# Kernel optimization log

Measured on AMD Instinct MI355X. Metric: run time of the kernel, lower is better.

The kernel has to match this reference:

```python
import jax, jax.numpy as jnp
import numpy as np

B, S, H = 2, 1024, 2048
KD = 32
N_CACHE = 16
RANKS = (4, 12, 40, 128)
SIM_THRESH = 0.95
CRIT_T, SIMPLE_T = 0.8, 0.3
EPS = 1e-8


def setup_inputs() -> dict:
    key = jax.random.key(0)
    ks = jax.random.split(key, 24)
    f32 = jnp.float32
    inp = {}
    inp['hidden_states'] = jax.random.normal(ks[0], (B, S, H), f32)
    # token importance scorer: Linear(H, H//4) -> ReLU -> Linear(H//4, 1)
    inp['scorer_w1'] = jax.random.normal(ks[1], (H // 4, H), f32) * 0.1
    inp['scorer_b1'] = jnp.zeros((H // 4,), f32)
    inp['scorer_w2'] = jax.random.normal(ks[2], (1, H // 4), f32) * 0.1
    inp['scorer_b2'] = jnp.zeros((1,), f32)
    inp['pos_importance'] = jnp.ones((1024,), f32)
    # orthogonal key projection [KD, H] (rows orthonormal)
    q, _ = jnp.linalg.qr(jax.random.normal(ks[3], (H, KD), f32))
    inp['key_proj_w'] = q.T
    # cached keys: per-batch-row L2-normalized then flattened, as in _compute_key
    ck = jax.random.normal(ks[4], (N_CACHE, B, KD), f32)
    ck = ck / jnp.linalg.norm(ck, axis=-1, keepdims=True)
    inp['cache_keys'] = ck.reshape(N_CACHE, B * KD)
    inp['cache_deltas'] = jax.random.normal(ks[5], (N_CACHE, B, S, H), f32) * 0.02
    # complexity estimator: Linear(H, 64) -> ReLU -> Linear(64, 4)
    inp['ce_w1'] = jax.random.normal(ks[6], (64, H), f32) * 0.02
    inp['ce_b1'] = jnp.zeros((64,), f32)
    inp['ce_w2'] = jax.random.normal(ks[7], (len(RANKS), 64), f32) * 0.02
    inp['ce_b2'] = jnp.zeros((len(RANKS),), f32)
    # adaptive low-rank U/V per rank option, init std=0.02
    for i, r in enumerate(RANKS):
        inp[f'u{r}'] = jax.random.normal(ks[8 + 2 * i], (r, H), f32) * 0.02
        inp[f'v{r}'] = jax.random.normal(ks[9 + 2 * i], (H, r), f32) * 0.02
    # dense stand-in for the wrapped original transformer layer
    inp['layer_w'] = jax.random.normal(ks[16], (H, H), f32) * 0.02
    inp['layer_b'] = jnp.zeros((H,), f32)
    return inp


def _forward(hidden_states, scorer_w1, scorer_b1, scorer_w2, scorer_b2,
             pos_importance, key_proj_w, cache_keys, cache_deltas,
             ce_w1, ce_b1, ce_w2, ce_b2,
             u4, v4, u12, v12, u40, v40, u128, v128,
             layer_w, layer_b):
    x = hidden_states
    Bn, Sn, _ = x.shape
    # ---- token importance scoring ----
    h = jax.nn.relu(jnp.einsum('bsh,fh->bsf', x, scorer_w1) + scorer_b1)
    content = jnp.einsum('bsf,of->bso', h, scorer_w2)[..., 0] + scorer_b2[0]  # [B,S]
    pos = pos_importance[:Sn][None, :]
    imp = jax.nn.sigmoid(content + 0.1 * pos)
    imp = imp.at[:, 0].multiply(2.0).at[:, -1].multiply(2.0)
    critical = imp > CRIT_T
    simple = imp < SIMPLE_T
    normal = ~(critical | simple)
    # ---- critical path: original layer on critically-masked input ----
    crit_in = jnp.where(critical[..., None], x, 0.0)
    crit_out = jnp.einsum('bsh,oh->bso', crit_in, layer_w) + layer_b
    # ---- simple path: batched 1-NN cosine cache lookup (replaces python loop) ----
    x_pooled = x.mean(axis=1)  # [B,H]
    qk = jax.lax.stop_gradient(x_pooled @ key_proj_w.T)  # no_grad in original
    qk = qk / jnp.maximum(jnp.linalg.norm(qk, axis=-1, keepdims=True), EPS)
    qf = qk.reshape(-1)  # flattened [B*KD], as F.cosine_similarity(dim=0)
    ck = jax.lax.stop_gradient(cache_keys)  # cached entries are detached
    sims = (ck @ qf) / (jnp.maximum(jnp.linalg.norm(ck, axis=-1), EPS)
                        * jnp.maximum(jnp.linalg.norm(qf), EPS))  # [N_CACHE]
    best = jnp.argmax(sims)
    hit = sims[best] >= SIM_THRESH
    cached_delta = jax.lax.stop_gradient(cache_deltas[best])  # [B,S,H]
    lr4 = (x @ u4.T) @ v4.T  # rank-4 update on cache miss
    simple_out = x + jnp.where(hit, cached_delta, lr4)
    # ---- normal path: adaptive-rank low-rank update ----
    ce_h = jax.nn.relu(jax.lax.stop_gradient(x_pooled) @ ce_w1.T + ce_b1)
    scores = ce_h @ ce_w2.T + ce_b2  # [B,4]
    rank_idx = jnp.argmax(scores.reshape(-1)) % len(RANKS)  # flat argmax as torch.argmax
    branches = [
        lambda xx: (xx @ u4.T) @ v4.T,
        lambda xx: (xx @ u12.T) @ v12.T,
        lambda xx: (xx @ u40.T) @ v40.T,
        lambda xx: (xx @ u128.T) @ v128.T,
    ]
    normal_update = jax.lax.switch(rank_idx, branches, x)
    normal_out = x + normal_update
    # ---- route per-token (masks partition all tokens) ----
    out = jnp.where(critical[..., None], crit_out,
          jnp.where(simple[..., None], simple_out, normal_out))
    return out


def reference(hidden_states, scorer_w1, scorer_b1, scorer_w2, scorer_b2,
              pos_importance, key_proj_w, cache_keys, cache_deltas,
              ce_w1, ce_b1, ce_w2, ce_b2,
              u4, v4, u12, v12, u40, v40, u128, v128,
              layer_w, layer_b):
    return _forward(hidden_states, scorer_w1, scorer_b1, scorer_w2, scorer_b2,
                    pos_importance, key_proj_w, cache_keys, cache_deltas,
                    ce_w1, ce_b1, ce_w2, ce_b2,
                    u4, v4, u12, v12, u40, v40, u128, v128,
                    layer_w, layer_b)
```

## Files before the change

### kernel.cpp

```cpp
#include <hip/hip_runtime.h>
#include <math.h>

#define B_  2
#define S_  1024
#define H_  2048
#define F_  512
#define KD_ 32
#define NC_ 16
#define M_  2048
#define NPROJ 184
#define LDP 192
#define KZ_ 4

typedef __attribute__((ext_vector_type(8))) short bf16x8;
typedef __attribute__((ext_vector_type(4))) float f32x4;

typedef __attribute__((address_space(1))) const void gvoid_t;
typedef __attribute__((address_space(3))) void lvoid_t;

__device__ __forceinline__ void gld16(const void* g, void* l) {
    __builtin_amdgcn_global_load_lds((gvoid_t*)g, (lvoid_t*)l, 16, 0, 0);
}

__device__ __forceinline__ ushort f2bf(float f) {
    unsigned u = __float_as_uint(f);
    u += 0x7FFFu + ((u >> 16) & 1u);
    return (ushort)(u >> 16);
}
__device__ __forceinline__ float bf2f(ushort h) {
    return __uint_as_float(((unsigned)h) << 16);
}
__device__ __forceinline__ uint4 pack_hi8(float4 a, float4 b) {
    uint4 r;
    r.x = (unsigned)f2bf(a.x) | ((unsigned)f2bf(a.y) << 16);
    r.y = (unsigned)f2bf(a.z) | ((unsigned)f2bf(a.w) << 16);
    r.z = (unsigned)f2bf(b.x) | ((unsigned)f2bf(b.y) << 16);
    r.w = (unsigned)f2bf(b.z) | ((unsigned)f2bf(b.w) << 16);
    return r;
}
__device__ __forceinline__ void pack_hilo8(float4 a, float4 b, uint4* hi, uint4* lo) {
    float v[8] = {a.x, a.y, a.z, a.w, b.x, b.y, b.z, b.w};
    unsigned h[8], l[8];
#pragma unroll
    for (int i = 0; i < 8; ++i) {
        ushort hh = f2bf(v[i]);
        h[i] = hh;
        l[i] = f2bf(v[i] - bf2f(hh));
    }
    *hi = make_uint4(h[0] | (h[1] << 16), h[2] | (h[3] << 16),
                     h[4] | (h[5] << 16), h[6] | (h[7] << 16));
    *lo = make_uint4(l[0] | (l[1] << 16), l[2] | (l[3] << 16),
                     l[4] | (l[5] << 16), l[6] | (l[7] << 16));
}

__global__ __launch_bounds__(256) void conv_kernel(
    const float* __restrict__ x, const float* __restrict__ lw,
    const float* __restrict__ sw1,
    const float* __restrict__ u4, const float* __restrict__ u12,
    const float* __restrict__ u40, const float* __restrict__ u128,
    ushort* __restrict__ xhi, ushort* __restrict__ xlo,
    ushort* __restrict__ lwh, ushort* __restrict__ swh,
    ushort* __restrict__ swl, ushort* __restrict__ ubh,
    float* __restrict__ partial) {
    int blk = blockIdx.x, tid = threadIdx.x;
    if (blk < 128) {
        int c0 = tid << 3;
        float cs0 = 0.f, cs1 = 0.f, cs2 = 0.f, cs3 = 0.f;
        float cs4 = 0.f, cs5 = 0.f, cs6 = 0.f, cs7 = 0.f;
        for (int r = 0; r < 16; ++r) {
            size_t off = (size_t)(blk * 16 + r) * H_ + c0;
            float4 a = *(const float4*)(x + off);
            float4 b = *(const float4*)(x + off + 4);
            cs0 += a.x; cs1 += a.y; cs2 += a.z; cs3 += a.w;
            cs4 += b.x; cs5 += b.y; cs6 += b.z; cs7 += b.w;
            uint4 hi, lo;
            pack_hilo8(a, b, &hi, &lo);
            *(uint4*)(xhi + off) = hi;
            *(uint4*)(xlo + off) = lo;
        }
        float* pr = partial + (size_t)blk * H_ + c0;
        pr[0] = cs0; pr[1] = cs1; pr[2] = cs2; pr[3] = cs3;
        pr[4] = cs4; pr[5] = cs5; pr[6] = cs6; pr[7] = cs7;
    } else if (blk < 1152) {
        size_t base = (size_t)(blk - 128) * 4096 + (size_t)tid * 16;
#pragma unroll
        for (int q = 0; q < 2; ++q) {
            size_t o = base + q * 8;
            float4 a = *(const float4*)(lw + o);
            float4 b = *(const float4*)(lw + o + 4);
            *(uint4*)(lwh + o) = pack_hi8(a, b);
        }
    } else if (blk < 1408) {
        size_t base = (size_t)(blk - 1152) * 4096 + (size_t)tid * 16;
#pragma unroll
        for (int q = 0; q < 2; ++q) {
            size_t o = base + q * 8;
            float4 a = *(const float4*)(sw1 + o);
            float4 b = *(const float4*)(sw1 + o + 4);
            uint4 hi, lo;
            pack_hilo8(a, b, &hi, &lo);
            *(uint4*)(swh + o) = hi;
            *(uint4*)(swl + o) = lo;
        }
    } else {
        const float* src; ushort* dst; int rel;
        if (blk < 1410)      { src = u4;   dst = ubh;            rel = blk - 1408; }
        else if (blk < 1416) { src = u12;  dst = ubh + 4 * H_;   rel = blk - 1410; }
        else if (blk < 1436) { src = u40;  dst = ubh + 16 * H_;  rel = blk - 1416; }
        else                 { src = u128; dst = ubh + 56 * H_;  rel = blk - 1436; }
        size_t base = (size_t)rel * 4096 + (size_t)tid * 16;
#pragma unroll
        for (int q = 0; q < 2; ++q) {
            size_t o = base + q * 8;
            float4 a = *(const float4*)(src + o);
            float4 b = *(const float4*)(src + o + 4);
            *(uint4*)(dst + o) = pack_hi8(a, b);
        }
    }
}

__global__ __launch_bounds__(256) void pool_final_kernel(
    const float* __restrict__ partial, float* __restrict__ xp) {
    int b = blockIdx.x >> 3, chunk = blockIdx.x & 7;
    int col = (chunk << 8) + threadIdx.x;
    float s = 0.f;
    for (int seg = 0; seg < 64; ++seg)
        s += partial[(size_t)(b * 64 + seg) * H_ + col];
    xp[b * H_ + col] = s * (1.0f / S_);
}

__global__ __launch_bounds__(256) void decide_dots(
    const float* __restrict__ xp, const float* __restrict__ kpw,
    const float* __restrict__ cw1, float* __restrict__ dots) {
    __shared__ float red[4];
    int o = blockIdx.x, tid = threadIdx.x;
    const float* xr;
    const float* wr;
    if (o < 64) {
        xr = xp + (o >> 5) * H_;
        wr = kpw + (size_t)(o & 31) * H_;
    } else {
        int o2 = o - 64;
        xr = xp + (o2 >> 6) * H_;
        wr = cw1 + (size_t)(o2 & 63) * H_;
    }
    int k0 = tid << 3;
    float4 xa = *(const float4*)(xr + k0);
    float4 xb = *(const float4*)(xr + k0 + 4);
    float4 wa = *(const float4*)(wr + k0);
    float4 wb = *(const float4*)(wr + k0 + 4);
    float s = xa.x * wa.x + xa.y * wa.y + xa.z * wa.z + xa.w * wa.w
            + xb.x * wb.x + xb.y * wb.y + xb.z * wb.z + xb.w * wb.w;
    for (int off = 32; off > 0; off >>= 1) s += __shfl_down(s, off, 64);
    if ((tid & 63) == 0) red[tid >> 6] = s;
    __syncthreads();
    if (tid == 0) dots[o] = red[0] + red[1] + red[2] + red[3];
}

__global__ __launch_bounds__(64) void decide_final(
    const float* __restrict__ dots, const float* __restrict__ ck,
    const float* __restrict__ cb1, const float* __restrict__ cw2,
    const float* __restrict__ cb2, int* __restrict__ flags) {
    __shared__ float qk_s[64], ce_s[128], sims_s[NC_], sc_s[8];
    __shared__ float qn_s;
    int tid = threadIdx.x;
    if (tid < 64) qk_s[tid] = dots[tid];
    if (tid < 64) {
        ce_s[tid]      = fmaxf(dots[64 + tid] + cb1[tid & 63], 0.f);
        ce_s[tid + 64] = fmaxf(dots[128 + tid] + cb1[tid & 63], 0.f);
    }
    __syncthreads();
    if (tid == 0) {
        for (int b = 0; b < B_; ++b) {
            float nn = 0.f;
            for (int d = 0; d < KD_; ++d) { float v = qk_s[b * KD_ + d]; nn += v * v; }
            float den = fmaxf(sqrtf(nn), 1e-8f);
            for (int d = 0; d < KD_; ++d) qk_s[b * KD_ + d] /= den;
        }
        float qn = 0.f;
        for (int i = 0; i < B_ * KD_; ++i) qn += qk_s[i] * qk_s[i];
        qn_s = fmaxf(sqrtf(qn), 1e-8f);
    }
    __syncthreads();
    if (tid < NC_) {
        float dot = 0.f, nn = 0.f;
        for (int i = 0; i < B_ * KD_; ++i) {
            float c = ck[tid * (B_ * KD_) + i];
            dot += c * qk_s[i]; nn += c * c;
        }
        sims_s[tid] = dot / (fmaxf(sqrtf(nn), 1e-8f) * qn_s);
    }
    if (tid >= 32 && tid < 40) {
        int p = tid - 32, b = p >> 2, o = p & 3;
        float v = cb2[o];
        for (int j = 0; j < 64; ++j) v += ce_s[b * 64 + j] * cw2[o * 64 + j];
        sc_s[p] = v;
    }
    __syncthreads();
    if (tid == 0) {
        float bestv = -1e30f; int best = 0;
        for (int n = 0; n < NC_; ++n)
            if (sims_s[n] > bestv) { bestv = sims_s[n]; best = n; }
        flags[2] = (bestv >= 0.95f) ? 1 : 0;
        flags[3] = best;
        float bs = -1e30f; int bi = 0;
        for (int p = 0; p < 8; ++p)
            if (sc_s[p] > bs) { bs = sc_s[p]; bi = p; }
        flags[1] = bi & 3;
    }
}

__global__ __launch_bounds__(256) void big_gemm(
    const ushort* __restrict__ xhi, const ushort* __restrict__ xlo,
    const ushort* __restrict__ swh, const ushort* __restrict__ swl,
    const ushort* __restrict__ ubh,
    float* __restrict__ Hp, float* __restrict__ Pp) {
    __shared__ ushort Ah[2][128][32], Al[2][128][32], Bh[2][128][32], Bl[2][128][32];
    int m0 = blockIdx.x << 7;
    int ny = blockIdx.y;
    int kz = blockIdx.z;
    bool split = ny < 4;
    int tid = threadIdx.x;
    int lr = tid >> 2;
    int lc = (tid & 3) << 3;

    const ushort* a0p = xhi + (size_t)(m0 + lr) * H_ + lc;
    const ushort* a1p = a0p + (size_t)64 * H_;
    const ushort* l0p = xlo + (size_t)(m0 + lr) * H_ + lc;
    const ushort* l1p = l0p + (size_t)64 * H_;
    const ushort* b0p; const ushort* b1p;
    const ushort* c0p = l0p; const ushort* c1p = l1p;
    if (split) {
        b0p = swh + (size_t)(ny * 128 + lr) * H_ + lc;
        b1p = b0p + (size_t)64 * H_;
        c0p = swl + (size_t)(ny * 128 + lr) * H_ + lc;
        c1p = c0p + (size_t)64 * H_;
    } else {
        b0p = ubh + (size_t)((ny - 4) * 128 + lr) * H_ + lc;
        b1p = b0p + (size_t)64 * H_;
    }

    int lane = tid & 63, w = tid >> 6;
    int wm = (w >> 1) << 6, wn = (w & 1) << 6;
    int fr = lane & 15, kb = (lane >> 4) << 3;

    f32x4 zero4 = {0.f, 0.f, 0.f, 0.f};
    f32x4 acc[4][4];
#pragma unroll
    for (int i = 0; i < 4; ++i)
#pragma unroll
        for (int j = 0; j < 4; ++j) acc[i][j] = zero4;

    int kbeg = kz << 9;

#define STAGE_BG(bb, k0)                                                  \
    do {                                                                  \
        gld16(a0p + (k0), &Ah[bb][lr][lc]);                               \
        gld16(a1p + (k0), &Ah[bb][lr + 64][lc]);                          \
        gld16(b0p + (k0), &Bh[bb][lr][lc]);                               \
        gld16(b1p + (k0), &Bh[bb][lr + 64][lc]);                          \
        if (split) {                                                      \
            gld16(l0p + (k0), &Al[bb][lr][lc]);                           \
            gld16(l1p + (k0), &Al[bb][lr + 64][lc]);                      \
            gld16(c0p + (k0), &Bl[bb][lr][lc]);                           \
            gld16(c1p + (k0), &Bl[bb][lr + 64][lc]);                      \
        }                                                                 \
    } while (0)

    STAGE_BG(0, kbeg);
    __syncthreads();
    int cur = 0;
    for (int kt = 0; kt < 16; ++kt) {
        if (kt + 1 < 16) STAGE_BG(cur ^ 1, kbeg + ((kt + 1) << 5));
        bf16x8 ah[4], bh4[4], al4[4], bl4[4];
#pragma unroll
        for (int mt = 0; mt < 4; ++mt)
            ah[mt] = *(const bf16x8*)&Ah[cur][wm + (mt << 4) + fr][kb];
#pragma unroll
        for (int nt = 0; nt < 4; ++nt)
            bh4[nt] = *(const bf16x8*)&Bh[cur][wn + (nt << 4) + fr][kb];
        if (split) {
#pragma unroll
            for (int mt = 0; mt < 4; ++mt)
                al4[mt] = *(const bf16x8*)&Al[cur][wm + (mt << 4) + fr][kb];
#pragma unroll
            for (int nt = 0; nt < 4; ++nt)
                bl4[nt] = *(const bf16x8*)&Bl[cur][wn + (nt << 4) + fr][kb];
        }
#pragma unroll
        for (int mt = 0; mt < 4; ++mt)
#pragma unroll
            for (int nt = 0; nt < 4; ++nt) {
                acc[mt][nt] = __builtin_amdgcn_mfma_f32_16x16x32_bf16(
                    ah[mt], bh4[nt], acc[mt][nt], 0, 0, 0);
                if (split) {
                    acc[mt][nt] = __builtin_amdgcn_mfma_f32_16x16x32_bf16(
                        ah[mt], bl4[nt], acc[mt][nt], 0, 0, 0);
                    acc[mt][nt] = __builtin_amdgcn_mfma_f32_16x16x32_bf16(
                        al4[mt], bh4[nt], acc[mt][nt], 0, 0, 0);
                }
            }
        __syncthreads();
        cur ^= 1;
    }
#undef STAGE_BG

    int orr = (lane >> 4) << 2;
    if (split) {
        float* dst = Hp + (size_t)kz * M_ * F_;
#pragma unroll
        for (int mt = 0; mt < 4; ++mt)
#pragma unroll
            for (int r = 0; r < 4; ++r) {
                int m = m0 + wm + (mt << 4) + orr + r;
                float* cr = dst + (size_t)m * F_ + (ny << 7) + wn;
#pragma unroll
                for (int nt = 0; nt < 4; ++nt)
                    cr[(nt << 4) + fr] = acc[mt][nt][r];
            }
    } else {
        float* dst = Pp + (size_t)kz * M_ * LDP;
        int nb0 = (ny - 4) << 7;
#pragma unroll
        for (int mt = 0; mt < 4; ++mt)
#pragma unroll
            for (int r = 0; r < 4; ++r) {
                int m = m0 + wm + (mt << 4) + orr + r;
                float* cr = dst + (size_t)m * LDP;
#pragma unroll
                for (int nt = 0; nt < 4; ++nt) {
                    int c = nb0 + wn + (nt << 4) + fr;
                    if (c < NPROJ) cr[c] = acc[mt][nt][r];
                }
            }
    }
}

__global__ __launch_bounds__(256) void route_kernel(
    const float* __restrict__ Hp, const float* __restrict__ sb1,
    const float* __restrict__ sw2, const float* __restrict__ sb2,
    const float* __restrict__ pos,
    int* __restrict__ flags, int* __restrict__ route, int* __restrict__ clist) {
    int tid = threadIdx.x;
    int m = (blockIdx.x << 2) + (tid >> 6);
    int lane = tid & 63;
    const float* h0 = Hp + (size_t)m * F_;
    const float* h1 = h0 + (size_t)M_ * F_;
    const float* h2 = h1 + (size_t)M_ * F_;
    const float* h3 = h2 + (size_t)M_ * F_;
    float s = 0.f;
    for (int f = lane; f < F_; f += 64)
        s += fmaxf(h0[f] + h1[f] + h2[f] + h3[f] + sb1[f], 0.f) * sw2[f];
    for (int off = 32; off > 0; off >>= 1) s += __shfl_down(s, off, 64);
    if (lane == 0) {
        float content = s + sb2[0];
        int si = m & (S_ - 1);
        float imp = 1.0f / (1.0f + expf(-(content + 0.1f * pos[si])));
        if (si == 0 || si == S_ - 1) imp *= 2.0f;
        int rt = (imp > 0.8f) ? 0 : ((imp < 0.3f) ? 1 : 2);
        route[m] = rt;
        if (rt == 0) {
            int idx = atomicAdd(&flags[0], 1);
            clist[idx] = m;
        }
    }
}

__global__ __launch_bounds__(256) void crit_gemm(
    const ushort* __restrict__ xhi, const ushort* __restrict__ lwh,
    const float* __restrict__ lb, const int* __restrict__ clist,
    const int* __restrict__ flags, float* __restrict__ out) {
    __shared__ ushort Ah[2][128][32], Bh[2][128][32];
    int M = flags[0];
    int m0 = blockIdx.x << 7;
    if (m0 >= M) return;
    int n0 = blockIdx.y << 7;
    int tid = threadIdx.x;
    int lr = tid >> 2, lc = (tid & 3) << 3;

    int gm0 = m0 + lr, gm1 = m0 + lr + 64;
    int ar0 = clist[gm0 < M ? gm0 : (M - 1)];
    int ar1 = clist[gm1 < M ? gm1 : (M - 1)];
    const ushort* a0p = xhi + (size_t)ar0 * H_ + lc;
    const ushort* a1p = xhi + (size_t)ar1 * H_ + lc;
    const ushort* b0p = lwh + (size_t)(n0 + lr) * H_ + lc;
    const ushort* b1p = b0p + (size_t)64 * H_;

    int lane = tid & 63, w = tid >> 6;
    int wm = (w >> 1) << 6, wn = (w & 1) << 6;
    int fr = lane & 15, kb = (lane >> 4) << 3;

    f32x4 zero4 = {0.f, 0.f, 0.f, 0.f};
    f32x4 acc[4][4];
#pragma unroll
    for (int i = 0; i < 4; ++i)
#pragma unroll
        for (int j = 0; j < 4; ++j) acc[i][j] = zero4;

#define STAGE_CG(bb, k0)                                                  \
    do {                                                                  \
        gld16(a0p + (k0), &Ah[bb][lr][lc]);                               \
        gld16(a1p + (k0), &Ah[bb][lr + 64][lc]);                          \
        gld16(b0p + (k0), &Bh[bb][lr][lc]);                               \
        gld16(b1p + (k0), &Bh[bb][lr + 64][lc]);                          \
    } while (0)

    STAGE_CG(0, 0);
    __syncthreads();
    int cur = 0;
    for (int kt = 0; kt < 64; ++kt) {
        if (kt + 1 < 64) STAGE_CG(cur ^ 1, (kt + 1) << 5);
        bf16x8 af[4], bf4[4];
#pragma unroll
        for (int mt = 0; mt < 4; ++mt)
            af[mt] = *(const bf16x8*)&Ah[cur][wm + (mt << 4) + fr][kb];
#pragma unroll
        for (int nt = 0; nt < 4; ++nt)
            bf4[nt] = *(const bf16x8*)&Bh[cur][wn + (nt << 4) + fr][kb];
#pragma unroll
        for (int mt = 0; mt < 4; ++mt)
#pragma unroll
            for (int nt = 0; nt < 4; ++nt)
                acc[mt][nt] = __builtin_amdgcn_mfma_f32_16x16x32_bf16(
                    af[mt], bf4[nt], acc[mt][nt], 0, 0, 0);
        __syncthreads();
        cur ^= 1;
    }
#undef STAGE_CG

    int orr = (lane >> 4) << 2;
#pragma unroll
    for (int mt = 0; mt < 4; ++mt)
#pragma unroll
        for (int r = 0; r < 4; ++r) {
            int m = m0 + wm + (mt << 4) + orr + r;
            if (m < M) {
                float* cr = out + (size_t)clist[m] * H_;
#pragma unroll
                for (int nt = 0; nt < 4; ++nt) {
                    int c = n0 + wn + (nt << 4) + fr;
                    cr[c] = acc[mt][nt][r] + lb[c];
                }
            }
        }
}

__global__ __launch_bounds__(256) void stage2_kernel(
    const float* __restrict__ x, const float* __restrict__ Pp,
    const float* __restrict__ v4, const float* __restrict__ v12,
    const float* __restrict__ v40, const float* __restrict__ v128,
    const float* __restrict__ cd, const int* __restrict__ flags,
    const int* __restrict__ route, float* __restrict__ out) {
    __shared__ float TsR[16][132];
    __shared__ float Ts4[16][4];
    __shared__ int rt_s[16];
    int tid = threadIdx.x;
    int m0 = (blockIdx.x >> 4) << 4;
    int c0 = (blockIdx.x & 15) << 7;

    if (tid < 16) rt_s[tid] = route[m0 + tid];
    int r = flags[1];
    const float* V = (r == 0) ? v4 : (r == 1) ? v12 : (r == 2) ? v40 : v128;
    int Kr  = (r == 0) ? 4 : (r == 1) ? 12 : (r == 2) ? 40 : 128;
    int off = (r == 0) ? 0 : (r == 1) ? 4  : (r == 2) ? 16 : 56;
    int hit = flags[2], best = flags[3];

    const float* Pp1 = Pp + (size_t)M_ * LDP;
    const float* Pp2 = Pp1 + (size_t)M_ * LDP;
    const float* Pp3 = Pp2 + (size_t)M_ * LDP;
    for (int idx = tid; idx < 16 * Kr; idx += 256) {
        int i = idx / Kr, j = idx - i * Kr;
        size_t o = (size_t)(m0 + i) * LDP + off + j;
        TsR[i][j] = Pp[o] + Pp1[o] + Pp2[o] + Pp3[o];
    }
    if (tid < 64) {
        int i = tid >> 2, j = tid & 3;
        size_t o = (size_t)(m0 + i) * LDP + j;
        Ts4[i][j] = Pp[o] + Pp1[o] + Pp2[o] + Pp3[o];
    }
    __syncthreads();
    bool any1 = false, any2 = false;
#pragma unroll
    for (int i = 0; i < 16; ++i) { any1 |= (rt_s[i] == 1); any2 |= (rt_s[i] == 2); }
    if (!any1 && !any2) return;
    bool need4 = any1 && !hit;

    int c = c0 + (tid & 127);
    int i0 = (tid >> 7) << 3;

    float aR[8];
#pragma unroll
    for (int i = 0; i < 8; ++i) aR[i] = 0.f;
    if (any2) {
        const float* vrow = V + (size_t)c * Kr;
        for (int j = 0; j < Kr; j += 4) {
            const float4 vv = *(const float4*)(vrow + j);
#pragma unroll
            for (int i = 0; i < 8; ++i) {
                const float4 tv = *(const float4*)&TsR[i0 + i][j];
                aR[i] += tv.x * vv.x + tv.y * vv.y + tv.z * vv.z + tv.w * vv.w;
            }
        }
    }
    float a4[8];
    if (need4) {
        const float4 vv = *(const float4*)(v4 + (size_t)c * 4);
#pragma unroll
        for (int i = 0; i < 8; ++i) {
            const float4 tv = *(const float4*)&Ts4[i0 + i][0];
            a4[i] = tv.x * vv.x + tv.y * vv.y + tv.z * vv.z + tv.w * vv.w;
        }
    }
#pragma unroll
    for (int i = 0; i < 8; ++i) {
        int rt = rt_s[i0 + i];
        if (rt == 0) continue;
        size_t o = (size_t)(m0 + i0 + i) * H_ + c;
        float upd;
        if (rt == 1)
            upd = hit ? cd[(size_t)best * (size_t)(M_ * H_) + o] : a4[i];
        else
            upd = aR[i];
        out[o] = x[o] + upd;
    }
}

extern "C" void kernel_launch(void* const* d_in, const int* in_sizes, int n_in,
                              void* d_out, int out_size, void* d_ws, size_t ws_size,
                              hipStream_t stream) {
    const float* x    = (const float*)d_in[0];
    const float* sw1  = (const float*)d_in[1];
    const float* sb1  = (const float*)d_in[2];
    const float* sw2  = (const float*)d_in[3];
    const float* sb2  = (const float*)d_in[4];
    const float* pos  = (const float*)d_in[5];
    const float* kpw  = (const float*)d_in[6];
    const float* ck   = (const float*)d_in[7];
    const float* cd   = (const float*)d_in[8];
    const float* cw1  = (const float*)d_in[9];
    const float* cb1  = (const float*)d_in[10];
    const float* cw2  = (const float*)d_in[11];
    const float* cb2  = (const float*)d_in[12];
    const float* u4   = (const float*)d_in[13];
    const float* v4   = (const float*)d_in[14];
    const float* u12  = (const float*)d_in[15];
    const float* v12  = (const float*)d_in[16];
    const float* u40  = (const float*)d_in[17];
    const float* v40  = (const float*)d_in[18];
    const float* u128 = (const float*)d_in[19];
    const float* v128 = (const float*)d_in[20];
    const float* lw   = (const float*)d_in[21];
    const float* lb   = (const float*)d_in[22];
    float* out = (float*)d_out;

    ushort* xhi = (ushort*)d_ws;
    ushort* xlo = xhi + (size_t)M_ * H_;
    ushort* lwh = xlo + (size_t)M_ * H_;
    ushort* swh = lwh + (size_t)H_ * H_;
    ushort* swl = swh + (size_t)F_ * H_;
    ushort* ubh = swl + (size_t)F_ * H_;
    float* fbase   = (float*)(ubh + (size_t)256 * H_);
    float* xp      = fbase;
    float* partial = xp + 2 * H_;
    float* Pp      = partial + 128 * H_;
    float* Hp      = Pp + (size_t)KZ_ * M_ * LDP;
    float* dots    = Hp + (size_t)KZ_ * M_ * F_;
    int*   flags   = (int*)(dots + 256);
    int*   route   = flags + 8;
    int*   clist   = route + M_;

    hipMemsetAsync(flags, 0, sizeof(int), stream);

    conv_kernel<<<1500, 256, 0, stream>>>(x, lw, sw1, u4, u12, u40, u128,
                                          xhi, xlo, lwh, swh, swl, ubh, partial);
    pool_final_kernel<<<16, 256, 0, stream>>>(partial, xp);
    decide_dots<<<192, 256, 0, stream>>>(xp, kpw, cw1, dots);
    decide_final<<<1, 64, 0, stream>>>(dots, ck, cb1, cw2, cb2, flags);
    big_gemm<<<dim3(16, 6, KZ_), 256, 0, stream>>>(xhi, xlo, swh, swl, ubh, Hp, Pp);
    route_kernel<<<512, 256, 0, stream>>>(Hp, sb1, sw2, sb2, pos,
                                          flags, route, clist);
    crit_gemm<<<dim3(16, 16), 256, 0, stream>>>(xhi, lwh, lb, clist, flags, out);
    stage2_kernel<<<2048, 256, 0, stream>>>(x, Pp, v4, v12, v40, v128,
                                            cd, flags, route, out);
}
```

Measured before the change: 519.0 us.

## Merge small decision kernels and fuse crit GEMM with stage2; swizzle LDS

Folds the pooling reduction into the dot-product kernel and moves the single-block decision logic into an extra block of the routing kernel. The critical-token GEMM and the stage2 update now run as one launch, with blocks split by index and sharing one shared-memory buffer. This cuts the launch count from eight to five and lets the two output-writing phases overlap. It also adds an XOR swizzle to the LDS column index in both GEMMs to reduce bank conflicts on the MFMA fragment reads. Each pooldots block now re-reads the full partial-sum buffer, so that redundant traffic is the cost.

Measured after the change: 479.6 us. 1.08x faster.

```diff
diff --git a/kernel.cpp b/kernel.cpp
--- a/kernel.cpp
+++ b/kernel.cpp
@@ -119,95 +119,41 @@
     }
 }
 
-__global__ __launch_bounds__(256) void pool_final_kernel(
-    const float* __restrict__ partial, float* __restrict__ xp) {
-    int b = blockIdx.x >> 3, chunk = blockIdx.x & 7;
-    int col = (chunk << 8) + threadIdx.x;
-    float s = 0.f;
-    for (int seg = 0; seg < 64; ++seg)
-        s += partial[(size_t)(b * 64 + seg) * H_ + col];
-    xp[b * H_ + col] = s * (1.0f / S_);
-}
-
-__global__ __launch_bounds__(256) void decide_dots(
-    const float* __restrict__ xp, const float* __restrict__ kpw,
+__global__ __launch_bounds__(256) void pooldots_kernel(
+    const float* __restrict__ partial, const float* __restrict__ kpw,
     const float* __restrict__ cw1, float* __restrict__ dots) {
     __shared__ float red[4];
     int o = blockIdx.x, tid = threadIdx.x;
-    const float* xr;
-    const float* wr;
+    int b; const float* wr;
     if (o < 64) {
-        xr = xp + (o >> 5) * H_;
+        b = o >> 5;
         wr = kpw + (size_t)(o & 31) * H_;
     } else {
         int o2 = o - 64;
-        xr = xp + (o2 >> 6) * H_;
+        b = o2 >> 6;
         wr = cw1 + (size_t)(o2 & 63) * H_;
     }
     int k0 = tid << 3;
-    float4 xa = *(const float4*)(xr + k0);
-    float4 xb = *(const float4*)(xr + k0 + 4);
+    float xs0 = 0.f, xs1 = 0.f, xs2 = 0.f, xs3 = 0.f;
+    float xs4 = 0.f, xs5 = 0.f, xs6 = 0.f, xs7 = 0.f;
+    const float* pb = partial + (size_t)b * 64 * H_ + k0;
+    for (int seg = 0; seg < 64; ++seg) {
+        float4 p0 = *(const float4*)(pb + (size_t)seg * H_);
+        float4 p1 = *(const float4*)(pb + (size_t)seg * H_ + 4);
+        xs0 += p0.x; xs1 += p0.y; xs2 += p0.z; xs3 += p0.w;
+        xs4 += p1.x; xs5 += p1.y; xs6 += p1.z; xs7 += p1.w;
+    }
+    const float inv = 1.0f / S_;
     float4 wa = *(const float4*)(wr + k0);
     float4 wb = *(const float4*)(wr + k0 + 4);
-    float s = xa.x * wa.x + xa.y * wa.y + xa.z * wa.z + xa.w * wa.w
-            + xb.x * wb.x + xb.y * wb.y + xb.z * wb.z + xb.w * wb.w;
+    float s = (xs0 * inv) * wa.x + (xs1 * inv) * wa.y
+            + (xs2 * inv) * wa.z + (xs3 * inv) * wa.w
+            + (xs4 * inv) * wb.x + (xs5 * inv) * wb.y
+            + (xs6 * inv) * wb.z + (xs7 * inv) * wb.w;
     for (int off = 32; off > 0; off >>= 1) s += __shfl_down(s, off, 64);
     if ((tid & 63) == 0) red[tid >> 6] = s;
     __syncthreads();
     if (tid == 0) dots[o] = red[0] + red[1] + red[2] + red[3];
-}
-
-__global__ __launch_bounds__(64) void decide_final(
-    const float* __restrict__ dots, const float* __restrict__ ck,
-    const float* __restrict__ cb1, const float* __restrict__ cw2,
-    const float* __restrict__ cb2, int* __restrict__ flags) {
-    __shared__ float qk_s[64], ce_s[128], sims_s[NC_], sc_s[8];
-    __shared__ float qn_s;
-    int tid = threadIdx.x;
-    if (tid < 64) qk_s[tid] = dots[tid];
-    if (tid < 64) {
-        ce_s[tid]      = fmaxf(dots[64 + tid] + cb1[tid & 63], 0.f);
-        ce_s[tid + 64] = fmaxf(dots[128 + tid] + cb1[tid & 63], 0.f);
-    }
-    __syncthreads();
-    if (tid == 0) {
-        for (int b = 0; b < B_; ++b) {
-            float nn = 0.f;
-            for (int d = 0; d < KD_; ++d) { float v = qk_s[b * KD_ + d]; nn += v * v; }
-            float den = fmaxf(sqrtf(nn), 1e-8f);
-            for (int d = 0; d < KD_; ++d) qk_s[b * KD_ + d] /= den;
-        }
-        float qn = 0.f;
-        for (int i = 0; i < B_ * KD_; ++i) qn += qk_s[i] * qk_s[i];
-        qn_s = fmaxf(sqrtf(qn), 1e-8f);
-    }
-    __syncthreads();
-    if (tid < NC_) {
-        float dot = 0.f, nn = 0.f;
-        for (int i = 0; i < B_ * KD_; ++i) {
-            float c = ck[tid * (B_ * KD_) + i];
-            dot += c * qk_s[i]; nn += c * c;
-        }
-        sims_s[tid] = dot / (fmaxf(sqrtf(nn), 1e-8f) * qn_s);
-    }
-    if (tid >= 32 && tid < 40) {
-        int p = tid - 32, b = p >> 2, o = p & 3;
-        float v = cb2[o];
-        for (int j = 0; j < 64; ++j) v += ce_s[b * 64 + j] * cw2[o * 64 + j];
-        sc_s[p] = v;
-    }
-    __syncthreads();
-    if (tid == 0) {
-        float bestv = -1e30f; int best = 0;
-        for (int n = 0; n < NC_; ++n)
-            if (sims_s[n] > bestv) { bestv = sims_s[n]; best = n; }
-        flags[2] = (bestv >= 0.95f) ? 1 : 0;
-        flags[3] = best;
-        float bs = -1e30f; int bi = 0;
-        for (int p = 0; p < 8; ++p)
-            if (sc_s[p] > bs) { bs = sc_s[p]; bi = p; }
-        flags[1] = bi & 3;
-    }
 }
 
 __global__ __launch_bounds__(256) void big_gemm(
@@ -223,26 +169,28 @@
     int tid = threadIdx.x;
     int lr = tid >> 2;
     int lc = (tid & 3) << 3;
-
-    const ushort* a0p = xhi + (size_t)(m0 + lr) * H_ + lc;
+    int lcs = lc ^ (((lr >> 1) & 3) << 3);
+
+    const ushort* a0p = xhi + (size_t)(m0 + lr) * H_ + lcs;
     const ushort* a1p = a0p + (size_t)64 * H_;
-    const ushort* l0p = xlo + (size_t)(m0 + lr) * H_ + lc;
+    const ushort* l0p = xlo + (size_t)(m0 + lr) * H_ + lcs;
     const ushort* l1p = l0p + (size_t)64 * H_;
     const ushort* b0p; const ushort* b1p;
     const ushort* c0p = l0p; const ushort* c1p = l1p;
     if (split) {
-        b0p = swh + (size_t)(ny * 128 + lr) * H_ + lc;
+        b0p = swh + (size_t)(ny * 128 + lr) * H_ + lcs;
         b1p = b0p + (size_t)64 * H_;
-        c0p = swl + (size_t)(ny * 128 + lr) * H_ + lc;
+        c0p = swl + (size_t)(ny * 128 + lr) * H_ + lcs;
         c1p = c0p + (size_t)64 * H_;
     } else {
-        b0p = ubh + (size_t)((ny - 4) * 128 + lr) * H_ + lc;
+        b0p = ubh + (size_t)((ny - 4) * 128 + lr) * H_ + lcs;
         b1p = b0p + (size_t)64 * H_;
     }
 
     int lane = tid & 63, w = tid >> 6;
     int wm = (w >> 1) << 6, wn = (w & 1) << 6;
-    int fr = lane & 15, kb = (lane >> 4) << 3;
+    int fr = lane & 15;
+    int kb = ((lane >> 4) << 3) ^ (((fr >> 1) & 3) << 3);
 
     f32x4 zero4 = {0.f, 0.f, 0.f, 0.f};
     f32x4 acc[4][4];
@@ -336,127 +284,186 @@
     }
 }
 
-__global__ __launch_bounds__(256) void route_kernel(
+__global__ __launch_bounds__(256) void routefinal_kernel(
     const float* __restrict__ Hp, const float* __restrict__ sb1,
     const float* __restrict__ sw2, const float* __restrict__ sb2,
     const float* __restrict__ pos,
+    const float* __restrict__ dots, const float* __restrict__ ck,
+    const float* __restrict__ cb1, const float* __restrict__ cw2,
+    const float* __restrict__ cb2,
     int* __restrict__ flags, int* __restrict__ route, int* __restrict__ clist) {
     int tid = threadIdx.x;
-    int m = (blockIdx.x << 2) + (tid >> 6);
-    int lane = tid & 63;
-    const float* h0 = Hp + (size_t)m * F_;
-    const float* h1 = h0 + (size_t)M_ * F_;
-    const float* h2 = h1 + (size_t)M_ * F_;
-    const float* h3 = h2 + (size_t)M_ * F_;
-    float s = 0.f;
-    for (int f = lane; f < F_; f += 64)
-        s += fmaxf(h0[f] + h1[f] + h2[f] + h3[f] + sb1[f], 0.f) * sw2[f];
-    for (int off = 32; off > 0; off >>= 1) s += __shfl_down(s, off, 64);
-    if (lane == 0) {
-        float content = s + sb2[0];
-        int si = m & (S_ - 1);
-        float imp = 1.0f / (1.0f + expf(-(content + 0.1f * pos[si])));
-        if (si == 0 || si == S_ - 1) imp *= 2.0f;
-        int rt = (imp > 0.8f) ? 0 : ((imp < 0.3f) ? 1 : 2);
-        route[m] = rt;
-        if (rt == 0) {
-            int idx = atomicAdd(&flags[0], 1);
-            clist[idx] = m;
-        }
-    }
-}
-
-__global__ __launch_bounds__(256) void crit_gemm(
+    if (blockIdx.x < 512) {
+        int m = ((int)blockIdx.x << 2) + (tid >> 6);
+        int lane = tid & 63;
+        const float* h0 = Hp + (size_t)m * F_;
+        const float* h1 = h0 + (size_t)M_ * F_;
+        const float* h2 = h1 + (size_t)M_ * F_;
+        const float* h3 = h2 + (size_t)M_ * F_;
+        float s = 0.f;
+        for (int f = lane; f < F_; f += 64)
+            s += fmaxf(h0[f] + h1[f] + h2[f] + h3[f] + sb1[f], 0.f) * sw2[f];
+        for (int off = 32; off > 0; off >>= 1) s += __shfl_down(s, off, 64);
+        if (lane == 0) {
+            float content = s + sb2[0];
+            int si = m & (S_ - 1);
+            float imp = 1.0f / (1.0f + expf(-(content + 0.1f * pos[si])));
+            if (si == 0 || si == S_ - 1) imp *= 2.0f;
+            int rt = (imp > 0.8f) ? 0 : ((imp < 0.3f) ? 1 : 2);
+            route[m] = rt;
+            if (rt == 0) {
+                int idx = atomicAdd(&flags[0], 1);
+                clist[idx] = m;
+            }
+        }
+        return;
+    }
+    __shared__ float qk_s[64], ce_s[128], sims_s[NC_], sc_s[8];
+    __shared__ float qn_s;
+    if (tid < 64) {
+        qk_s[tid]      = dots[tid];
+        ce_s[tid]      = fmaxf(dots[64 + tid] + cb1[tid & 63], 0.f);
+        ce_s[tid + 64] = fmaxf(dots[128 + tid] + cb1[tid & 63], 0.f);
+    }
+    __syncthreads();
+    if (tid == 0) {
+        for (int b = 0; b < B_; ++b) {
+            float nn = 0.f;
+            for (int d = 0; d < KD_; ++d) { float v = qk_s[b * KD_ + d]; nn += v * v; }
+            float den = fmaxf(sqrtf(nn), 1e-8f);
+            for (int d = 0; d < KD_; ++d) qk_s[b * KD_ + d] /= den;
+        }
+        float qn = 0.f;
+        for (int i = 0; i < B_ * KD_; ++i) qn += qk_s[i] * qk_s[i];
+        qn_s = fmaxf(sqrtf(qn), 1e-8f);
+    }
+    __syncthreads();
+    if (tid < NC_) {
+        float dot = 0.f, nn = 0.f;
+        for (int i = 0; i < B_ * KD_; ++i) {
+            float c = ck[tid * (B_ * KD_) + i];
+            dot += c * qk_s[i]; nn += c * c;
+        }
+        sims_s[tid] = dot / (fmaxf(sqrtf(nn), 1e-8f) * qn_s);
+    }
+    if (tid >= 32 && tid < 40) {
+        int p = tid - 32, b = p >> 2, o = p & 3;
+        float v = cb2[o];
+        for (int j = 0; j < 64; ++j) v += ce_s[b * 64 + j] * cw2[o * 64 + j];
+        sc_s[p] = v;
+    }
+    __syncthreads();
+    if (tid == 0) {
+        float bestv = -1e30f; int best = 0;
+        for (int n = 0; n < NC_; ++n)
+            if (sims_s[n] > bestv) { bestv = sims_s[n]; best = n; }
+        flags[2] = (bestv >= 0.95f) ? 1 : 0;
+        flags[3] = best;
+        float bs = -1e30f; int bi = 0;
+        for (int p = 0; p < 8; ++p)
+            if (sc_s[p] > bs) { bs = sc_s[p]; bi = p; }
+        flags[1] = bi & 3;
+    }
+}
+
+__global__ __launch_bounds__(256) void critstage2_kernel(
     const ushort* __restrict__ xhi, const ushort* __restrict__ lwh,
-    const float* __restrict__ lb, const int* __restrict__ clist,
-    const int* __restrict__ flags, float* __restrict__ out) {
-    __shared__ ushort Ah[2][128][32], Bh[2][128][32];
-    int M = flags[0];
-    int m0 = blockIdx.x << 7;
-    if (m0 >= M) return;
-    int n0 = blockIdx.y << 7;
-    int tid = threadIdx.x;
-    int lr = tid >> 2, lc = (tid & 3) << 3;
-
-    int gm0 = m0 + lr, gm1 = m0 + lr + 64;
-    int ar0 = clist[gm0 < M ? gm0 : (M - 1)];
-    int ar1 = clist[gm1 < M ? gm1 : (M - 1)];
-    const ushort* a0p = xhi + (size_t)ar0 * H_ + lc;
-    const ushort* a1p = xhi + (size_t)ar1 * H_ + lc;
-    const ushort* b0p = lwh + (size_t)(n0 + lr) * H_ + lc;
-    const ushort* b1p = b0p + (size_t)64 * H_;
-
-    int lane = tid & 63, w = tid >> 6;
-    int wm = (w >> 1) << 6, wn = (w & 1) << 6;
-    int fr = lane & 15, kb = (lane >> 4) << 3;
-
-    f32x4 zero4 = {0.f, 0.f, 0.f, 0.f};
-    f32x4 acc[4][4];
-#pragma unroll
-    for (int i = 0; i < 4; ++i)
-#pragma unroll
-        for (int j = 0; j < 4; ++j) acc[i][j] = zero4;
-
-#define STAGE_CG(bb, k0)                                                  \
-    do {                                                                  \
-        gld16(a0p + (k0), &Ah[bb][lr][lc]);                               \
-        gld16(a1p + (k0), &Ah[bb][lr + 64][lc]);                          \
-        gld16(b0p + (k0), &Bh[bb][lr][lc]);                               \
-        gld16(b1p + (k0), &Bh[bb][lr + 64][lc]);                          \
-    } while (0)
-
-    STAGE_CG(0, 0);
-    __syncthreads();
-    int cur = 0;
-    for (int kt = 0; kt < 64; ++kt) {
-        if (kt + 1 < 64) STAGE_CG(cur ^ 1, (kt + 1) << 5);
-        bf16x8 af[4], bf4[4];
-#pragma unroll
-        for (int mt = 0; mt < 4; ++mt)
-            af[mt] = *(const bf16x8*)&Ah[cur][wm + (mt << 4) + fr][kb];
-#pragma unroll
-        for (int nt = 0; nt < 4; ++nt)
-            bf4[nt] = *(const bf16x8*)&Bh[cur][wn + (nt << 4) + fr][kb];
-#pragma unroll
-        for (int mt = 0; mt < 4; ++mt)
-#pragma unroll
-            for (int nt = 0; nt < 4; ++nt)
-                acc[mt][nt] = __builtin_amdgcn_mfma_f32_16x16x32_bf16(
-                    af[mt], bf4[nt], acc[mt][nt], 0, 0, 0);
-        __syncthreads();
-        cur ^= 1;
-    }
-#undef STAGE_CG
-
-    int orr = (lane >> 4) << 2;
-#pragma unroll
-    for (int mt = 0; mt < 4; ++mt)
-#pragma unroll
-        for (int r = 0; r < 4; ++r) {
-            int m = m0 + wm + (mt << 4) + orr + r;
-            if (m < M) {
-                float* cr = out + (size_t)clist[m] * H_;
-#pragma unroll
-                for (int nt = 0; nt < 4; ++nt) {
-                    int c = n0 + wn + (nt << 4) + fr;
-                    cr[c] = acc[mt][nt][r] + lb[c];
-                }
-            }
-        }
-}
-
-__global__ __launch_bounds__(256) void stage2_kernel(
+    const float* __restrict__ lb,
     const float* __restrict__ x, const float* __restrict__ Pp,
     const float* __restrict__ v4, const float* __restrict__ v12,
     const float* __restrict__ v40, const float* __restrict__ v128,
     const float* __restrict__ cd, const int* __restrict__ flags,
-    const int* __restrict__ route, float* __restrict__ out) {
-    __shared__ float TsR[16][132];
-    __shared__ float Ts4[16][4];
-    __shared__ int rt_s[16];
+    const int* __restrict__ route, const int* __restrict__ clist,
+    float* __restrict__ out) {
+    __shared__ __align__(16) char smem[32768];
+    int bi = blockIdx.x;
     int tid = threadIdx.x;
-    int m0 = (blockIdx.x >> 4) << 4;
-    int c0 = (blockIdx.x & 15) << 7;
+
+    if (bi < 256) {
+        ushort* As = (ushort*)smem;
+        ushort* Bs = As + 8192;
+        int M = flags[0];
+        int m0 = (bi >> 4) << 7;
+        if (m0 >= M) return;
+        int n0 = (bi & 15) << 7;
+        int lr = tid >> 2, lc = (tid & 3) << 3;
+        int lcs = lc ^ (((lr >> 1) & 3) << 3);
+
+        int gm0 = m0 + lr, gm1 = m0 + lr + 64;
+        int ar0 = clist[gm0 < M ? gm0 : (M - 1)];
+        int ar1 = clist[gm1 < M ? gm1 : (M - 1)];
+        const ushort* a0p = xhi + (size_t)ar0 * H_ + lcs;
+        const ushort* a1p = xhi + (size_t)ar1 * H_ + lcs;
+        const ushort* b0p = lwh + (size_t)(n0 + lr) * H_ + lcs;
+        const ushort* b1p = b0p + (size_t)64 * H_;
+
+        int lane = tid & 63, w = tid >> 6;
+        int wm = (w >> 1) << 6, wn = (w & 1) << 6;
+        int fr = lane & 15;
+        int kb = ((lane >> 4) << 3) ^ (((fr >> 1) & 3) << 3);
+
+        f32x4 zero4 = {0.f, 0.f, 0.f, 0.f};
+        f32x4 acc[4][4];
+#pragma unroll
+        for (int i = 0; i < 4; ++i)
+#pragma unroll
+            for (int j = 0; j < 4; ++j) acc[i][j] = zero4;
+
+#define STAGE_CG(bb, k0)                                                  \
+        do {                                                              \
+            gld16(a0p + (k0), &As[(bb) * 4096 + lr * 32 + lc]);           \
+            gld16(a1p + (k0), &As[(bb) * 4096 + (lr + 64) * 32 + lc]);    \
+            gld16(b0p + (k0), &Bs[(bb) * 4096 + lr * 32 + lc]);           \
+            gld16(b1p + (k0), &Bs[(bb) * 4096 + (lr + 64) * 32 + lc]);    \
+        } while (0)
+
+        STAGE_CG(0, 0);
+        __syncthreads();
+        int cur = 0;
+        for (int kt = 0; kt < 64; ++kt) {
+            if (kt + 1 < 64) STAGE_CG(cur ^ 1, (kt + 1) << 5);
+            bf16x8 af[4], bf4[4];
+#pragma unroll
+            for (int mt = 0; mt < 4; ++mt)
+                af[mt] = *(const bf16x8*)&As[cur * 4096 + (wm + (mt << 4) + fr) * 32 + kb];
+#pragma unroll
+            for (int nt = 0; nt < 4; ++nt)
+                bf4[nt] = *(const bf16x8*)&Bs[cur * 4096 + (wn + (nt << 4) + fr) * 32 + kb];
+#pragma unroll
+            for (int mt = 0; mt < 4; ++mt)
+#pragma unroll
+                for (int nt = 0; nt < 4; ++nt)
+                    acc[mt][nt] = __builtin_amdgcn_mfma_f32_16x16x32_bf16(
+                        af[mt], bf4[nt], acc[mt][nt], 0, 0, 0);
+            __syncthreads();
+            cur ^= 1;
+        }
+#undef STAGE_CG
+
+        int orr = (lane >> 4) << 2;
+#pragma unroll
+        for (int mt = 0; mt < 4; ++mt)
+#pragma unroll
+            for (int r = 0; r < 4; ++r) {
+                int m = m0 + wm + (mt << 4) + orr + r;
+                if (m < M) {
+                    float* cr = out + (size_t)clist[m] * H_;
+#pragma unroll
+                    for (int nt = 0; nt < 4; ++nt) {
+                        int c = n0 + wn + (nt << 4) + fr;
+                        cr[c] = acc[mt][nt][r] + lb[c];
+                    }
+                }
+            }
+        return;
+    }
+
+    float* TsR = (float*)smem;
+    float* Ts4 = TsR + 16 * 132;
+    int*   rt_s = (int*)(Ts4 + 64);
+    int sb = bi - 256;
+    int m0 = (sb >> 4) << 4;
+    int c0 = (sb & 15) << 7;
 
     if (tid < 16) rt_s[tid] = route[m0 + tid];
     int r = flags[1];
@@ -471,12 +478,12 @@
     for (int idx = tid; idx < 16 * Kr; idx += 256) {
         int i = idx / Kr, j = idx - i * Kr;
         size_t o = (size_t)(m0 + i) * LDP + off + j;
-        TsR[i][j] = Pp[o] + Pp1[o] + Pp2[o] + Pp3[o];
+        TsR[i * 132 + j] = Pp[o] + Pp1[o] + Pp2[o] + Pp3[o];
     }
     if (tid < 64) {
         int i = tid >> 2, j = tid & 3;
         size_t o = (size_t)(m0 + i) * LDP + j;
-        Ts4[i][j] = Pp[o] + Pp1[o] + Pp2[o] + Pp3[o];
+        Ts4[i * 4 + j] = Pp[o] + Pp1[o] + Pp2[o] + Pp3[o];
     }
     __syncthreads();
     bool any1 = false, any2 = false;
@@ -497,7 +504,7 @@
             const float4 vv = *(const float4*)(vrow + j);
 #pragma unroll
             for (int i = 0; i < 8; ++i) {
-                const float4 tv = *(const float4*)&TsR[i0 + i][j];
+                const float4 tv = *(const float4*)&TsR[(i0 + i) * 132 + j];
                 aR[i] += tv.x * vv.x + tv.y * vv.y + tv.z * vv.z + tv.w * vv.w;
             }
         }
@@ -507,7 +514,7 @@
         const float4 vv = *(const float4*)(v4 + (size_t)c * 4);
 #pragma unroll
         for (int i = 0; i < 8; ++i) {
-            const float4 tv = *(const float4*)&Ts4[i0 + i][0];
+            const float4 tv = *(const float4*)&Ts4[(i0 + i) * 4];
             a4[i] = tv.x * vv.x + tv.y * vv.y + tv.z * vv.z + tv.w * vv.w;
         }
     }
@@ -560,8 +567,7 @@
     ushort* swl = swh + (size_t)F_ * H_;
     ushort* ubh = swl + (size_t)F_ * H_;
     float* fbase   = (float*)(ubh + (size_t)256 * H_);
-    float* xp      = fbase;
-    float* partial = xp + 2 * H_;
+    float* partial = fbase;
     float* Pp      = partial + 128 * H_;
     float* Hp      = Pp + (size_t)KZ_ * M_ * LDP;
     float* dots    = Hp + (size_t)KZ_ * M_ * F_;
@@ -573,13 +579,12 @@
 
     conv_kernel<<<1500, 256, 0, stream>>>(x, lw, sw1, u4, u12, u40, u128,
                                           xhi, xlo, lwh, swh, swl, ubh, partial);
-    pool_final_kernel<<<16, 256, 0, stream>>>(partial, xp);
-    decide_dots<<<192, 256, 0, stream>>>(xp, kpw, cw1, dots);
-    decide_final<<<1, 64, 0, stream>>>(dots, ck, cb1, cw2, cb2, flags);
+    pooldots_kernel<<<192, 256, 0, stream>>>(partial, kpw, cw1, dots);
     big_gemm<<<dim3(16, 6, KZ_), 256, 0, stream>>>(xhi, xlo, swh, swl, ubh, Hp, Pp);
-    route_kernel<<<512, 256, 0, stream>>>(Hp, sb1, sw2, sb2, pos,
-                                          flags, route, clist);
-    crit_gemm<<<dim3(16, 16), 256, 0, stream>>>(xhi, lwh, lb, clist, flags, out);
-    stage2_kernel<<<2048, 256, 0, stream>>>(x, Pp, v4, v12, v40, v128,
-                                            cd, flags, route, out);
-}
+    routefinal_kernel<<<513, 256, 0, stream>>>(Hp, sb1, sw2, sb2, pos,
+                                               dots, ck, cb1, cw2, cb2,
+                                               flags, route, clist);
+    critstage2_kernel<<<2304, 256, 0, stream>>>(xhi, lwh, lb, x, Pp,
+                                                v4, v12, v40, v128,
+                                                cd, flags, route, clist, out);
+}
```
